# Optimization experiments

Measured on AMD Instinct MI355X. Metric: run time of the kernel, lower is better.

The kernel has to match this reference:

```python
import math
import jax, jax.numpy as jnp
import numpy as np

D_MODEL, N_HEADS, QKV, D_HEAD, D_FF, N_BLOCKS, IN_DIM = 288, 8, 328, 41, 1315, 4, 83
B, S = 1024, 128
EPS = 1e-5


def setup_inputs() -> dict:
    key = jax.random.key(0)
    ks = iter(jax.random.split(key, 64))
    def rn(shape, scale=0.05):
        return jax.random.normal(next(ks), shape, jnp.float32) * scale
    inp = {
        "x": jax.random.normal(next(ks), (B, S, IN_DIM), jnp.float32),
        "Wp": rn((D_MODEL, IN_DIM)), "bp": rn((D_MODEL,)),
        "phase": rn((D_MODEL,)),
        "Wq": rn((N_BLOCKS, QKV, D_MODEL)), "bq": rn((N_BLOCKS, QKV)),
        "Wk": rn((N_BLOCKS, QKV, D_MODEL)), "bk": rn((N_BLOCKS, QKV)),
        "Wv": rn((N_BLOCKS, QKV, D_MODEL)), "bv": rn((N_BLOCKS, QKV)),
        "Wo": rn((N_BLOCKS, D_MODEL, QKV)), "bo": rn((N_BLOCKS, D_MODEL)),
        "temp": jnp.ones((N_BLOCKS,), jnp.float32) + rn((N_BLOCKS,), 0.01),
        "qscale": jnp.ones((N_BLOCKS, N_HEADS), jnp.float32) + rn((N_BLOCKS, N_HEADS), 0.01),
        "Wf1": rn((N_BLOCKS, D_FF, D_MODEL)), "bf1": rn((N_BLOCKS, D_FF)),
        "Wf2": rn((N_BLOCKS, D_MODEL, D_FF)), "bf2": rn((N_BLOCKS, D_MODEL)),
        "n1w": jnp.ones((N_BLOCKS, D_MODEL), jnp.float32), "n1b": jnp.zeros((N_BLOCKS, D_MODEL), jnp.float32),
        "n2w": jnp.ones((N_BLOCKS, D_MODEL), jnp.float32), "n2b": jnp.zeros((N_BLOCKS, D_MODEL), jnp.float32),
        "skip": jnp.ones((N_BLOCKS,), jnp.float32),
        "bn_w": jnp.ones((D_MODEL,), jnp.float32), "bn_b": jnp.zeros((D_MODEL,), jnp.float32),
        "bn_mean": rn((D_MODEL,)), "bn_var": jax.random.uniform(next(ks), (D_MODEL,), jnp.float32, 0.5, 1.5),
        "h1w": rn((144, D_MODEL)), "h1b": rn((144,)),
        "h2w": rn((72, 144)), "h2b": rn((72,)),
        "h3w": rn((1, 72)), "h3b": rn((1,)),
        "u1w": rn((72, D_MODEL)), "u1b": rn((72,)),
        "u2w": rn((1, 72)), "u2b": rn((1,)),
    }
    return inp


def _layer_norm(x, w, b):
    mu = jnp.mean(x, axis=-1, keepdims=True)
    var = jnp.mean((x - mu) ** 2, axis=-1, keepdims=True)
    return (x - mu) * jax.lax.rsqrt(var + EPS) * w + b


def reference(x, Wp, bp, phase, Wq, bq, Wk, bk, Wv, bv, Wo, bo, temp, qscale,
              Wf1, bf1, Wf2, bf2, n1w, n1b, n2w, n2b, skip,
              bn_w, bn_b, bn_mean, bn_var,
              h1w, h1b, h2w, h2b, h3w, h3b, u1w, u1b, u2w, u2b):
    Bsz, Sl, _ = x.shape
    # input projection
    h = jnp.einsum('bsi,di->bsd', x, Wp) + bp
    # sinusoidal positional encoding modulated by cos(quantum_phase)
    pos = jnp.arange(Sl, dtype=jnp.float32)[:, None]
    div = jnp.exp(jnp.arange(0, D_MODEL, 2, dtype=jnp.float32) * (-math.log(10000.0) / D_MODEL))
    pe = jnp.zeros((Sl, D_MODEL), jnp.float32)
    pe = pe.at[:, 0::2].set(jnp.sin(pos * div)).at[:, 1::2].set(jnp.cos(pos * div))
    h = h + pe * jnp.cos(phase)

    for l in range(N_BLOCKS):
        # attention with temperature-scaled softmax + post-softmax per-head scale
        q = (jnp.einsum('bsd,qd->bsq', h, Wq[l]) + bq[l]).reshape(Bsz, Sl, N_HEADS, D_HEAD)
        k = (jnp.einsum('bsd,qd->bsq', h, Wk[l]) + bk[l]).reshape(Bsz, Sl, N_HEADS, D_HEAD)
        v = (jnp.einsum('bsd,qd->bsq', h, Wv[l]) + bv[l]).reshape(Bsz, Sl, N_HEADS, D_HEAD)
        scale = math.sqrt(D_HEAD) * temp[l]
        scores = jnp.einsum('bqhd,bkhd->bhqk', q, k) / scale  # [B,H,S,S]
        attn = jax.nn.softmax(scores, axis=-1) * qscale[l][None, :, None, None]
        o = jnp.einsum('bhqk,bkhd->bqhd', attn, v).reshape(Bsz, Sl, QKV)
        o = jnp.einsum('bsq,dq->bsd', o, Wo[l]) + bo[l]
        h = _layer_norm(h + skip[l] * o, n1w[l], n1b[l])
        # GELU FFN (exact erf gelu, dropout inactive in eval)
        f = jax.nn.gelu(jnp.einsum('bsd,fd->bsf', h, Wf1[l]) + bf1[l], approximate=False)
        f = jnp.einsum('bsf,df->bsd', f, Wf2[l]) + bf2[l]
        h = _layer_norm(h + f, n2w[l], n2b[l])

    pooled = jnp.mean(h, axis=1)  # [B, D_MODEL]
    # output head: BatchNorm1d (eval, running stats) -> GELU -> MLP
    z = (pooled - bn_mean) * jax.lax.rsqrt(bn_var + EPS) * bn_w + bn_b
    z = jax.nn.gelu(z, approximate=False)
    z = jax.nn.gelu(z @ h1w.T + h1b, approximate=False)
    z = jax.nn.gelu(z @ h2w.T + h2b, approximate=False)
    pred = z @ h3w.T + h3b  # [B, 1]
    # uncertainty head
    u = jax.nn.relu(pooled @ u1w.T + u1b)
    unc = jax.nn.softplus(u @ u2w.T + u2b)  # [B, 1]
    return pred, unc
```

## Files before the change

kernel.cpp:

```cpp
#include <hip/hip_runtime.h>
#include <cstdint>

typedef __attribute__((ext_vector_type(8))) short short8;
typedef __attribute__((ext_vector_type(4))) short s4v;
typedef __attribute__((ext_vector_type(4))) float floatx4;

#define DEV __device__ __forceinline__

DEV short f2bf(float f) {
  unsigned u = __builtin_bit_cast(unsigned, f);
  u += 0x7fffu + ((u >> 16) & 1u);
  return (short)(u >> 16);
}
DEV short f2bf_ru(float f) {
  unsigned u = __builtin_bit_cast(unsigned, f);
  return (short)((u + 0x8000u) >> 16);
}
DEV float bf2f(short s) {
  unsigned u = ((unsigned)(unsigned short)s) << 16;
  return __builtin_bit_cast(float, u);
}
DEV float gelu_exact(float x) {
  return 0.5f * x * (1.0f + erff(x * 0.70710678118654752f));
}
DEV float gelu_fast(float x) {
  const float t2 = 1.5957691216057308f * (x + 0.044715f * x * x * x);
  return x / (1.0f + __expf(-t2));
}
DEV void gload16(const void* g, void* l) {
  __builtin_amdgcn_global_load_lds((const __attribute__((address_space(1))) void*)g,
                                   (__attribute__((address_space(3))) void*)l,
                                   16, 0, 0);
}

template<int MODE>
__global__ __launch_bounds__(256)
void gemm_kernel(const short* __restrict__ A, const short* __restrict__ Bw,
                 const float* __restrict__ bias, short* __restrict__ C,
                 const float* __restrict__ pe,
                 int K, int lda, int ldb, int ldc, int Nstore, int NT, long hstride)
{
  __shared__ __align__(16) short lds[128 * 136];
  short* As = lds;
  short* Bs = lds + 128 * 32;
  short* Ct = lds;

  const int tid  = threadIdx.x;
  const int wave = tid >> 6, lane = tid & 63;
  const int quad = lane >> 4, r16 = lane & 15;
  const int per = gridDim.x >> 3;
  const int gti = (blockIdx.x & 7) * per + (blockIdx.x >> 3);
  const int mt = gti / NT, nt = gti - mt * NT;
  const int wm = (wave >> 1) * 64, wn = (wave & 1) * 64;

  const long Abase = (long)mt * 128 * lda;
  const long Bbase = (long)nt * 128 * ldb;

  const int row0 = tid >> 2,         cc0 = (tid & 3) ^ ((row0 >> 1) & 3);
  const int row1 = (256 + tid) >> 2, cc1 = ((256 + tid) & 3) ^ ((row1 >> 1) & 3);

  floatx4 acc[4][4] = {};

  for (int k0 = 0; k0 < K; k0 += 32) {
    __syncthreads();
    gload16(A  + Abase + (long)row0 * lda + k0 + cc0 * 8, &As[(0 * 256 + wave * 64) * 8]);
    gload16(A  + Abase + (long)row1 * lda + k0 + cc1 * 8, &As[(1 * 256 + wave * 64) * 8]);
    gload16(Bw + Bbase + (long)row0 * ldb + k0 + cc0 * 8, &Bs[(0 * 256 + wave * 64) * 8]);
    gload16(Bw + Bbase + (long)row1 * ldb + k0 + cc1 * 8, &Bs[(1 * 256 + wave * 64) * 8]);
    __syncthreads();

    short8 af[4], bfr[4];
#pragma unroll
    for (int i = 0; i < 4; ++i) {
      const int R = wm + i * 16 + r16;
      af[i] = *(const short8*)&As[R * 32 + (quad ^ ((R >> 1) & 3)) * 8];
    }
#pragma unroll
    for (int j = 0; j < 4; ++j) {
      const int R = wn + j * 16 + r16;
      bfr[j] = *(const short8*)&Bs[R * 32 + (quad ^ ((R >> 1) & 3)) * 8];
    }
#pragma unroll
    for (int i = 0; i < 4; ++i)
#pragma unroll
      for (int j = 0; j < 4; ++j)
        acc[i][j] = __builtin_amdgcn_mfma_f32_16x16x32_bf16(bfr[j], af[i], acc[i][j], 0, 0, 0);
  }

  const int mb0 = mt * 128, tb = nt * 128;

  __syncthreads();
#pragma unroll
  for (int j = 0; j < 4; ++j) {
    const int n0 = wn + j * 16 + quad * 4;
    const floatx4 b4 = *(const floatx4*)&bias[tb + n0];
#pragma unroll
    for (int i = 0; i < 4; ++i) {
      const int m = wm + i * 16 + r16;
      floatx4 v = acc[i][j] + b4;
      if (MODE == 1) {
#pragma unroll
        for (int rg = 0; rg < 4; ++rg) v[rg] = gelu_fast(v[rg]);
      }
      if (MODE == 2) {
        const floatx4 p4 = *(const floatx4*)&pe[((mb0 + m) & 127) * 384 + tb + n0];
        v = v + p4;
      }
      s4v o4;
#pragma unroll
      for (int rg = 0; rg < 4; ++rg) o4[rg] = f2bf_ru(v[rg]);
      *(s4v*)&Ct[m * 136 + n0] = o4;
    }
  }
  __syncthreads();

#pragma unroll
  for (int rr = 0; rr < 8; ++rr) {
    const int chunk = rr * 256 + tid;
    const int row = chunk >> 4, ch = chunk & 15;
    const int gcol = tb + ch * 8;
    if (MODE == 3) {
      const int g = gcol / 48, d0 = gcol - g * 48;
      *(short8*)(C + (long)g * hstride + (long)(mb0 + row) * 48 + d0) =
          *(const short8*)&Ct[row * 136 + ch * 8];
    } else if (gcol < Nstore) {
      *(short8*)(C + (long)(mb0 + row) * ldc + gcol) = *(const short8*)&Ct[row * 136 + ch * 8];
    }
  }
}

template<bool AHEAD>
__global__ __launch_bounds__(512, 4)
void gemm_ln_kernel(const short* __restrict__ A, const short* __restrict__ Bw,
                    const float* __restrict__ bias, short* __restrict__ h,
                    const float* __restrict__ lnw, const float* __restrict__ lnb,
                    const float* __restrict__ skip_p, int layer, int use_skip,
                    int K, int lda, int ldb, long ahs)
{
  __shared__ __align__(16) short lds[128 * 296];
  __shared__ float redp[4][2][2][16];
  __shared__ float reds[4][2][2][16];
  short* Hs = lds;

  const int tid  = threadIdx.x;
  const int wave = tid >> 6, lane = tid & 63;
  const int quad = lane >> 4, r16 = lane & 15;
  const int wr = wave >> 1, wc = wave & 1;
  const int mt = blockIdx.x;
  const long mrow0 = (long)mt * 128;

  floatx4 acc[2][9] = {};

  auto stage = [&](short* buf, int k0) {
    for (int c = tid; c < 1664; c += 512) {
      const void* src;
      if (c < 512) {
        const int row = c >> 2, cc = (c & 3) ^ ((row >> 1) & 3);
        if (AHEAD) {
          const int kc = k0 + cc * 8;
          const int g = kc / 48, d = kc - g * 48;
          src = A + (long)g * ahs + (mrow0 + row) * 48 + d;
        } else {
          src = A + (mrow0 + row) * lda + k0 + cc * 8;
        }
      } else {
        const int cb = c - 512;
        const int row = cb >> 2, cc = (cb & 3) ^ ((row >> 1) & 3);
        src = Bw + (long)row * ldb + k0 + cc * 8;
      }
      gload16(src, &buf[(size_t)(c & ~63) * 8]);
    }
  };

  auto compute = [&](const short* buf) {
    const short* As_ = buf;
    const short* Bs_ = buf + 4096;
    const int Ra0 = wr * 32 + r16, Ra1 = Ra0 + 16;
    const short8 af0 = *(const short8*)&As_[Ra0 * 32 + (quad ^ ((Ra0 >> 1) & 3)) * 8];
    const short8 af1 = *(const short8*)&As_[Ra1 * 32 + (quad ^ ((Ra1 >> 1) & 3)) * 8];
#pragma unroll
    for (int t = 0; t < 9; ++t) {
      const int Rb = wc * 144 + t * 16 + r16;
      const short8 b = *(const short8*)&Bs_[Rb * 32 + (quad ^ ((Rb >> 1) & 3)) * 8];
      acc[0][t] = __builtin_amdgcn_mfma_f32_16x16x32_bf16(b, af0, acc[0][t], 0, 0, 0);
      acc[1][t] = __builtin_amdgcn_mfma_f32_16x16x32_bf16(b, af1, acc[1][t], 0, 0, 0);
    }
  };

  short* const B0 = lds;
  short* const B1 = lds + 13312;

  stage(B0, 0);
  __syncthreads();
  int k0 = 0;
  while (true) {
    if (k0 + 32 < K) stage(B1, k0 + 32);
    compute(B0);
    __syncthreads();
    k0 += 32;
    if (k0 >= K) break;
    if (k0 + 32 < K) stage(B0, k0 + 32);
    compute(B1);
    __syncthreads();
    k0 += 32;
    if (k0 >= K) break;
  }

  for (int c = tid; c < 4608; c += 512) {
    const int row = c / 36, ch = c - row * 36;
    *(short8*)&Hs[row * 296 + ch * 8] =
        *(const short8*)(h + (mrow0 + row) * 288 + ch * 8);
  }
  __syncthreads();

  const float skipv = use_skip ? skip_p[layer] : 1.0f;
  const int m0 = wr * 32 + r16, m1 = m0 + 16;

  float ps0 = 0.f, ss0 = 0.f, ps1 = 0.f, ss1 = 0.f;
#pragma unroll
  for (int t = 0; t < 9; ++t) {
    const int n0 = wc * 144 + t * 16 + quad * 4;
    const floatx4 b4 = *(const floatx4*)&bias[n0];
    const s4v h40 = *(const s4v*)&Hs[m0 * 296 + n0];
    const s4v h41 = *(const s4v*)&Hs[m1 * 296 + n0];
#pragma unroll
    for (int rg = 0; rg < 4; ++rg) {
      const float y0 = bf2f(h40[rg]) + skipv * (acc[0][t][rg] + b4[rg]);
      const float y1 = bf2f(h41[rg]) + skipv * (acc[1][t][rg] + b4[rg]);
      acc[0][t][rg] = y0; acc[1][t][rg] = y1;
      ps0 += y0; ss0 += y0 * y0;
      ps1 += y1; ss1 += y1 * y1;
    }
  }
  ps0 += __shfl_xor(ps0, 16); ps0 += __shfl_xor(ps0, 32);
  ss0 += __shfl_xor(ss0, 16); ss0 += __shfl_xor(ss0, 32);
  ps1 += __shfl_xor(ps1, 16); ps1 += __shfl_xor(ps1, 32);
  ss1 += __shfl_xor(ss1, 16); ss1 += __shfl_xor(ss1, 32);
  if (lane < 16) {
    redp[wr][wc][0][r16] = ps0; redp[wr][wc][1][r16] = ps1;
    reds[wr][wc][0][r16] = ss0; reds[wr][wc][1][r16] = ss1;
  }
  __syncthreads();
  const float psum0 = redp[wr][0][0][r16] + redp[wr][1][0][r16];
  const float psum1 = redp[wr][0][1][r16] + redp[wr][1][1][r16];
  const float ssum0 = reds[wr][0][0][r16] + reds[wr][1][0][r16];
  const float ssum1 = reds[wr][0][1][r16] + reds[wr][1][1][r16];
  const float mean0 = psum0 * (1.f / 288.f), mean1 = psum1 * (1.f / 288.f);
  const float rstd0 = rsqrtf(ssum0 * (1.f / 288.f) - mean0 * mean0 + 1e-5f);
  const float rstd1 = rsqrtf(ssum1 * (1.f / 288.f) - mean1 * mean1 + 1e-5f);

#pragma unroll
  for (int t = 0; t < 9; ++t) {
    const int n0 = wc * 144 + t * 16 + quad * 4;
    const floatx4 w4 = *(const floatx4*)&lnw[n0];
    const floatx4 l4 = *(const floatx4*)&lnb[n0];
    s4v o0, o1;
#pragma unroll
    for (int rg = 0; rg < 4; ++rg) {
      o0[rg] = f2bf_ru((acc[0][t][rg] - mean0) * rstd0 * w4[rg] + l4[rg]);
      o1[rg] = f2bf_ru((acc[1][t][rg] - mean1) * rstd1 * w4[rg] + l4[rg]);
    }
    *(s4v*)&Hs[m0 * 296 + n0] = o0;
    *(s4v*)&Hs[m1 * 296 + n0] = o1;
  }
  __syncthreads();

  for (int c = tid; c < 4608; c += 512) {
    const int row = c / 36, ch = c - row * 36;
    *(short8*)(h + (mrow0 + row) * 288 + ch * 8) =
        *(const short8*)&Hs[row * 296 + ch * 8];
  }
}

__global__ __launch_bounds__(512, 2)
void ffn_kernel(short* __restrict__ h,
                const short* __restrict__ W1, const float* __restrict__ b1,
                const short* __restrict__ W2, const float* __restrict__ b2,
                const float* __restrict__ lnw, const float* __restrict__ lnb)
{
  __shared__ __align__(16) short lds[128 * 296];
  __shared__ float redp[4][2][2][16];
  __shared__ float reds[4][2][2][16];
  short* const fl = lds + 18432;

  const int tid  = threadIdx.x;
  const int wave = tid >> 6, lane = tid & 63;
  const int quad = lane >> 4, r16 = lane & 15;
  const int wr = wave >> 1, wp = wave & 1;
  const long mrow0 = (long)blockIdx.x * 128;

  short8 ha[2][9];
#pragma unroll
  for (int i = 0; i < 2; ++i) {
    const long rb = (mrow0 + wr * 32 + i * 16 + r16) * 288L;
#pragma unroll
    for (int k9 = 0; k9 < 9; ++k9)
      ha[i][k9] = *(const short8*)(h + rb + k9 * 32 + quad * 8);
  }

  floatx4 acc2[2][9] = {};

  const int srow = tid >> 2, scc = (tid & 3) ^ ((srow >> 1) & 3);

  auto stageW1 = [&](int c, int k9, short* dst) {
    gload16(W1 + ((long)(c * 128 + srow)) * 288 + k9 * 32 + scc * 8,
            &dst[(size_t)(tid & ~63) * 8]);
  };
  auto stageW2 = [&](int c, int ks, short* dst) {
    for (int c2 = tid; c2 < 1152; c2 += 512) {
      const int row = c2 >> 2, cc = (c2 & 3) ^ ((row >> 1) & 3);
      gload16(W2 + (long)row * 1408 + c * 128 + ks * 32 + cc * 8,
              &dst[(size_t)(c2 & ~63) * 8]);
    }
  };

  stageW1(0, 0, lds);
  __syncthreads();
  int cur = 0;

  for (int c = 0; c < 11; ++c) {
    floatx4 acc1[2][4] = {};

#pragma unroll
    for (int k9 = 0; k9 < 9; ++k9) {
      short* const Sn = lds + (cur ^ 1) * 9216;
      if (k9 < 8) stageW1(c, k9 + 1, Sn);
      else        stageW2(c, 0, Sn);

      const short* Sc = lds + cur * 9216;
      short8 bfr[4];
#pragma unroll
      for (int j = 0; j < 4; ++j) {
        const int R = wp * 64 + j * 16 + r16;
        bfr[j] = *(const short8*)&Sc[R * 32 + (quad ^ ((R >> 1) & 3)) * 8];
      }
#pragma unroll
      for (int i = 0; i < 2; ++i)
#pragma unroll
        for (int j = 0; j < 4; ++j)
          acc1[i][j] = __builtin_amdgcn_mfma_f32_16x16x32_bf16(bfr[j], ha[i][k9], acc1[i][j], 0, 0, 0);

      if (k9 == 8) {
#pragma unroll
        for (int i = 0; i < 2; ++i) {
          const int m = wr * 32 + i * 16 + r16;
#pragma unroll
          for (int j = 0; j < 4; ++j) {
            const int nb = c * 128 + wp * 64 + j * 16 + quad * 4;
            const floatx4 b4 = *(const floatx4*)&b1[nb];
            s4v o;
#pragma unroll
            for (int rg = 0; rg < 4; ++rg)
              o[rg] = f2bf_ru(gelu_fast(acc1[i][j][rg] + b4[rg]));
            const int ks = wp * 2 + (j >> 1);
            const int mg = ((j & 1) * 2 + (quad >> 1)) ^ ((m >> 1) & 3);
            *(s4v*)&fl[ks * 4096 + m * 32 + mg * 8 + (quad & 1) * 4] = o;
          }
        }
      }
      __syncthreads();
      cur ^= 1;
    }

#pragma unroll
    for (int ks = 0; ks < 4; ++ks) {
      short* const Sn = lds + (cur ^ 1) * 9216;
      if (ks < 3)      stageW2(c, ks + 1, Sn);
      else if (c < 10) stageW1(c + 1, 0, Sn);

      const short* Sc = lds + cur * 9216;
      short8 af2[2], br[9];
#pragma unroll
      for (int i = 0; i < 2; ++i) {
        const int R = wr * 32 + i * 16 + r16;
        af2[i] = *(const short8*)&fl[ks * 4096 + R * 32 + (quad ^ ((R >> 1) & 3)) * 8];
      }
#pragma unroll
      for (int t = 0; t < 9; ++t) {
        const int R = wp * 144 + t * 16 + r16;
        br[t] = *(const short8*)&Sc[R * 32 + (quad ^ ((R >> 1) & 3)) * 8];
      }
#pragma unroll
      for (int i = 0; i < 2; ++i)
#pragma unroll
        for (int t = 0; t < 9; ++t)
          acc2[i][t] = __builtin_amdgcn_mfma_f32_16x16x32_bf16(br[t], af2[i], acc2[i][t], 0, 0, 0);

      __syncthreads();
      cur ^= 1;
    }
  }

  for (int c2 = tid; c2 < 4608; c2 += 512) {
    const int row = c2 / 36, ch = c2 - row * 36;
    *(short8*)&lds[row * 296 + ch * 8] =
        *(const short8*)(h + (mrow0 + row) * 288 + ch * 8);
  }
  __syncthreads();

  const int m0 = wr * 32 + r16, m1 = m0 + 16;
  float ps0 = 0.f, ss0 = 0.f, ps1 = 0.f, ss1 = 0.f;
#pragma unroll
  for (int t = 0; t < 9; ++t) {
    const int n0 = wp * 144 + t * 16 + quad * 4;
    const floatx4 b4 = *(const floatx4*)&b2[n0];
    const s4v h40 = *(const s4v*)&lds[m0 * 296 + n0];
    const s4v h41 = *(const s4v*)&lds[m1 * 296 + n0];
#pragma unroll
    for (int rg = 0; rg < 4; ++rg) {
      const float y0 = bf2f(h40[rg]) + acc2[0][t][rg] + b4[rg];
      const float y1 = bf2f(h41[rg]) + acc2[1][t][rg] + b4[rg];
      acc2[0][t][rg] = y0; acc2[1][t][rg] = y1;
      ps0 += y0; ss0 += y0 * y0;
      ps1 += y1; ss1 += y1 * y1;
    }
  }
  ps0 += __shfl_xor(ps0, 16); ps0 += __shfl_xor(ps0, 32);
  ss0 += __shfl_xor(ss0, 16); ss0 += __shfl_xor(ss0, 32);
  ps1 += __shfl_xor(ps1, 16); ps1 += __shfl_xor(ps1, 32);
  ss1 += __shfl_xor(ss1, 16); ss1 += __shfl_xor(ss1, 32);
  if (lane < 16) {
    redp[wr][wp][0][r16] = ps0; redp[wr][wp][1][r16] = ps1;
    reds[wr][wp][0][r16] = ss0; reds[wr][wp][1][r16] = ss1;
  }
  __syncthreads();
  const float psum0 = redp[wr][0][0][r16] + redp[wr][1][0][r16];
  const float psum1 = redp[wr][0][1][r16] + redp[wr][1][1][r16];
  const float ssum0 = reds[wr][0][0][r16] + reds[wr][1][0][r16];
  const float ssum1 = reds[wr][0][1][r16] + reds[wr][1][1][r16];
  const float mean0 = psum0 * (1.f / 288.f), mean1 = psum1 * (1.f / 288.f);
  const float rstd0 = rsqrtf(ssum0 * (1.f / 288.f) - mean0 * mean0 + 1e-5f);
  const float rstd1 = rsqrtf(ssum1 * (1.f / 288.f) - mean1 * mean1 + 1e-5f);

#pragma unroll
  for (int t = 0; t < 9; ++t) {
    const int n0 = wp * 144 + t * 16 + quad * 4;
    const floatx4 w4 = *(const floatx4*)&lnw[n0];
    const floatx4 l4 = *(const floatx4*)&lnb[n0];
    s4v o0, o1;
#pragma unroll
    for (int rg = 0; rg < 4; ++rg) {
      o0[rg] = f2bf_ru((acc2[0][t][rg] - mean0) * rstd0 * w4[rg] + l4[rg]);
      o1[rg] = f2bf_ru((acc2[1][t][rg] - mean1) * rstd1 * w4[rg] + l4[rg]);
    }
    *(s4v*)&lds[m0 * 296 + n0] = o0;
    *(s4v*)&lds[m1 * 296 + n0] = o1;
  }
  __syncthreads();

  for (int c2 = tid; c2 < 4608; c2 += 512) {
    const int row = c2 / 36, ch = c2 - row * 36;
    *(short8*)(h + (mrow0 + row) * 288 + ch * 8) =
        *(const short8*)&lds[row * 296 + ch * 8];
  }
}

__global__ __launch_bounds__(256)
void attn_kernel(short* __restrict__ qkv,
                 const float* __restrict__ qscale, int layer, long Mc)
{
  __shared__ __align__(16) short qk[2 * 128 * 72];
  __shared__ __align__(16) short vsT[48 * 136 + 32];
  __shared__ float red[2][2][64];

  short* qs = qk;
  short* ks = qk + 128 * 72;
  short* Pb = qk;

  const int b = blockIdx.x, h = blockIdx.y;
  const int tid = threadIdx.x;
  const long sec = Mc * 48;
  const short* qg = qkv + (long)h * sec + (long)b * 128 * 48;
  const short* kg = qg + 8 * sec;
  const short* vg = qg + 16 * sec;
  short* og = qkv + (long)(16 + h) * sec + (long)b * 128 * 48;

  for (int c = tid; c < 768; c += 256) {
    const int s = c / 6, dc = c - (c / 6) * 6;
    *(short8*)&qs[s * 72 + dc * 8] = *(const short8*)(qg + (long)s * 48 + dc * 8);
    *(short8*)&ks[s * 72 + dc * 8] = *(const short8*)(kg + (long)s * 48 + dc * 8);
  }
  {
    short8 z;
#pragma unroll
    for (int j = 0; j < 8; ++j) z[j] = 0;
    for (int c = tid; c < 384; c += 256) {
      const int s = c / 3, t = c - (c / 3) * 3;
      *(short8*)&qs[s * 72 + 48 + t * 8] = z;
      *(short8*)&ks[s * 72 + 48 + t * 8] = z;
    }
  }
  for (int c = tid; c < 768; c += 256) {
    const int s = c & 127, dc = c >> 7;
    const short8 tv = *(const short8*)(vg + (long)s * 48 + dc * 8);
#pragma unroll
    for (int j = 0; j < 8; ++j) {
      const int row = dc * 8 + j;
      vsT[row * 136 + ((row >> 3) & 3) * 8 + s] = tv[j];
    }
  }
  __syncthreads();

  const int wave = tid >> 6, lane = tid & 63;
  const int quad = lane >> 4, r16 = lane & 15;
  const int wm = (wave >> 1) * 64, wn = (wave & 1) * 64;
  const int rh = wave >> 1, ch = wave & 1;
  const float qsc = qscale[layer * 8 + h];

  floatx4 acc[4][4] = {};
#pragma unroll
  for (int kk = 0; kk < 2; ++kk) {
    const int k0 = kk * 32;
    short8 af[4], bfr[4];
#pragma unroll
    for (int i = 0; i < 4; ++i)
      af[i] = *(const short8*)&qs[(wm + i * 16 + r16) * 72 + k0 + quad * 8];
#pragma unroll
    for (int j = 0; j < 4; ++j)
      bfr[j] = *(const short8*)&ks[(wn + j * 16 + r16) * 72 + k0 + quad * 8];
#pragma unroll
    for (int i = 0; i < 4; ++i)
#pragma unroll
      for (int j = 0; j < 4; ++j)
        acc[i][j] = __builtin_amdgcn_mfma_f32_16x16x32_bf16(bfr[j], af[i], acc[i][j], 0, 0, 0);
  }

  float rmax[4], rsum[4];
#pragma unroll
  for (int i = 0; i < 4; ++i) {
    float m = acc[i][0][0];
#pragma unroll
    for (int j = 0; j < 4; ++j)
#pragma unroll
      for (int rg = 0; rg < 4; ++rg) m = fmaxf(m, acc[i][j][rg]);
    m = fmaxf(m, __shfl_xor(m, 16));
    m = fmaxf(m, __shfl_xor(m, 32));
    rmax[i] = m;
  }
  if (lane < 16)
#pragma unroll
    for (int i = 0; i < 4; ++i) red[rh][ch][i * 16 + r16] = rmax[i];
  __syncthreads();
#pragma unroll
  for (int i = 0; i < 4; ++i)
    rmax[i] = fmaxf(red[rh][0][i * 16 + r16], red[rh][1][i * 16 + r16]);

#pragma unroll
  for (int i = 0; i < 4; ++i) {
    float s = 0.f;
#pragma unroll
    for (int j = 0; j < 4; ++j)
#pragma unroll
      for (int rg = 0; rg < 4; ++rg) {
        const float e = __expf(acc[i][j][rg] - rmax[i]);
        acc[i][j][rg] = e;
        s += e;
      }
    s += __shfl_xor(s, 16);
    s += __shfl_xor(s, 32);
    rsum[i] = s;
  }
  __syncthreads();
  if (lane < 16)
#pragma unroll
    for (int i = 0; i < 4; ++i) red[rh][ch][i * 16 + r16] = rsum[i];
  __syncthreads();
#pragma unroll
  for (int i = 0; i < 4; ++i)
    rmax[i] = qsc / (red[rh][0][i * 16 + r16] + red[rh][1][i * 16 + r16]);

#pragma unroll
  for (int i = 0; i < 4; ++i) {
    const int sq = wm + i * 16 + r16;
#pragma unroll
    for (int j = 0; j < 4; ++j) {
      const int sk0 = wn + j * 16 + quad * 4;
      s4v p4;
#pragma unroll
      for (int rg = 0; rg < 4; ++rg) p4[rg] = f2bf_ru(acc[i][j][rg] * rmax[i]);
      *(s4v*)&Pb[sq * 136 + sk0] = p4;
    }
  }
  __syncthreads();

  const int om = (wave >> 1) * 64, on = (wave & 1) * 32;
  const int jn = (on == 0) ? 2 : 1;
  floatx4 oacc[4][2] = {};
  for (int kk = 0; kk < 4; ++kk) {
    const int k0 = kk * 32;
    short8 af[4], bfr[2];
#pragma unroll
    for (int i = 0; i < 4; ++i)
      af[i] = *(const short8*)&Pb[(om + i * 16 + r16) * 136 + k0 + quad * 8];
    for (int j = 0; j < jn; ++j) {
      const int row = on + j * 16 + r16;
      bfr[j] = *(const short8*)&vsT[row * 136 + ((row >> 3) & 3) * 8 + k0 + quad * 8];
    }
#pragma unroll
    for (int i = 0; i < 4; ++i)
      for (int j = 0; j < jn; ++j)
        oacc[i][j] = __builtin_amdgcn_mfma_f32_16x16x32_bf16(bfr[j], af[i], oacc[i][j], 0, 0, 0);
  }
#pragma unroll
  for (int i = 0; i < 4; ++i)
    for (int j = 0; j < jn; ++j) {
      const int d0 = on + j * 16 + quad * 4;
      const int sq = om + i * 16 + r16;
      s4v o4;
#pragma unroll
      for (int rg = 0; rg < 4; ++rg) o4[rg] = f2bf_ru(oacc[i][j][rg]);
      *(s4v*)(og + (long)sq * 48 + d0) = o4;
    }
}

__global__ __launch_bounds__(256)
void head_kernel(const short* __restrict__ hb, float* __restrict__ out,
                 const float* bn_w, const float* bn_b, const float* bn_mean, const float* bn_var,
                 const float* h1w, const float* h1b, const float* h2w, const float* h2b,
                 const float* h3w, const float* h3b,
                 const float* u1w, const float* u1b, const float* u2w, const float* u2b)
{
  __shared__ float psum[252][8];
  __shared__ float pooled[288], z[288], z1[144], z2[72], uu[72];
  const int b = blockIdx.x, tid = threadIdx.x;

  if (tid < 252) {
    const int cch = tid % 36, grp = tid / 36;
    float a[8];
#pragma unroll
    for (int j = 0; j < 8; ++j) a[j] = 0.f;
    for (int r = grp; r < 128; r += 7) {
      const short8 hv = *(const short8*)(hb + ((long)b * 128 + r) * 288 + cch * 8);
#pragma unroll
      for (int j = 0; j < 8; ++j) a[j] += bf2f(hv[j]);
    }
#pragma unroll
    for (int j = 0; j < 8; ++j) psum[tid][j] = a[j];
  }
  __syncthreads();
  for (int d = tid; d < 288; d += 256) {
    const int cch = d >> 3, j = d & 7;
    float s = 0.f;
#pragma unroll
    for (int g = 0; g < 7; ++g) s += psum[g * 36 + cch][j];
    pooled[d] = s * (1.f / 128.f);
  }
  __syncthreads();

  for (int d = tid; d < 288; d += 256) {
    const float p = pooled[d];
    z[d] = gelu_exact((p - bn_mean[d]) * rsqrtf(bn_var[d] + 1e-5f) * bn_w[d] + bn_b[d]);
  }
  __syncthreads();

  if (tid < 144) {
    float s = h1b[tid];
    for (int k = 0; k < 288; ++k) s += z[k] * h1w[tid * 288 + k];
    z1[tid] = gelu_exact(s);
  } else if (tid < 216) {
    const int t = tid - 144;
    float s = u1b[t];
    for (int k = 0; k < 288; ++k) s += pooled[k] * u1w[t * 288 + k];
    uu[t] = fmaxf(s, 0.f);
  }
  __syncthreads();

  if (tid < 72) {
    float s = h2b[tid];
    for (int k = 0; k < 144; ++k) s += z1[k] * h2w[tid * 144 + k];
    z2[tid] = gelu_exact(s);
  }
  __syncthreads();

  if (tid == 0) {
    float s = h3b[0];
    for (int k = 0; k < 72; ++k) s += z2[k] * h3w[k];
    out[b] = s;
  }
  if (tid == 64) {
    float s = u2b[0];
    for (int k = 0; k < 72; ++k) s += uu[k] * u2w[k];
    out[1024 + b] = (s > 20.f) ? s : log1pf(__expf(s));
  }
}

__global__ void conv_w_kernel(const float* __restrict__ src, short* __restrict__ dst,
                              int N, int K, int Npad, int Kpad, int total)
{
  const int i = blockIdx.x * 256 + threadIdx.x;
  if (i >= total) return;
  const int kk = i % Kpad;
  const int t  = i / Kpad;
  const int n  = t % Npad;
  const int l  = t / Npad;
  const float v = (n < N && kk < K) ? src[((long)l * N + n) * K + kk] : 0.f;
  dst[i] = f2bf(v);
}

__global__ void conv_b_kernel(const float* __restrict__ src, float* __restrict__ dst,
                              int N, int Npad, int total)
{
  const int i = blockIdx.x * 256 + threadIdx.x;
  if (i >= total) return;
  const int n = i % Npad, l = i / Npad;
  dst[i] = (n < N) ? src[l * N + n] : 0.f;
}

__global__ void conv_wqkv_kernel(const float* __restrict__ Wq, const float* __restrict__ Wk,
                                 const float* __restrict__ Wv, const float* __restrict__ temp,
                                 short* __restrict__ dst)
{
  const int i = blockIdx.x * 256 + threadIdx.x;
  if (i >= 4 * 1152 * 288) return;
  const int kk = i % 288;
  const int t  = i / 288;
  const int r  = t % 1152;
  const int l  = t / 1152;
  const int g  = r / 48, d = r - (r / 48) * 48;
  const int sec = g >> 3, head = g & 7;
  float v = 0.f;
  if (d < 41) {
    const float* W = (sec == 0) ? Wq : (sec == 1) ? Wk : Wv;
    v = W[((long)l * 328 + head * 41 + d) * 288 + kk];
    if (sec == 0) v *= 1.0f / (6.4031242374328485f * temp[l]);
  }
  dst[i] = f2bf(v);
}

__global__ void conv_bqkv_kernel(const float* __restrict__ bq, const float* __restrict__ bk,
                                 const float* __restrict__ bv, const float* __restrict__ temp,
                                 float* __restrict__ dst)
{
  const int i = blockIdx.x * 256 + threadIdx.x;
  if (i >= 4 * 1152) return;
  const int r = i % 1152, l = i / 1152;
  const int g = r / 48, d = r - (r / 48) * 48;
  const int sec = g >> 3, head = g & 7;
  float v = 0.f;
  if (d < 41) {
    const float* b = (sec == 0) ? bq : (sec == 1) ? bk : bv;
    v = b[l * 328 + head * 41 + d];
    if (sec == 0) v *= 1.0f / (6.4031242374328485f * temp[l]);
  }
  dst[i] = v;
}

__global__ void conv_wo_kernel(const float* __restrict__ Wo, short* __restrict__ dst)
{
  const int i = blockIdx.x * 256 + threadIdx.x;
  if (i >= 4 * 288 * 384) return;
  const int kk = i % 384;
  const int t  = i / 384;
  const int n  = t % 288;
  const int l  = t / 288;
  const int head = kk / 48, d = kk - head * 48;
  float v = 0.f;
  if (d < 41) v = Wo[((long)l * 288 + n) * 328 + head * 41 + d];
  dst[i] = f2bf(v);
}

__global__ void conv_x_kernel(const float* __restrict__ x, short* __restrict__ xb, int total)
{
  const int i = blockIdx.x * 256 + threadIdx.x;
  if (i >= total) return;
  const int c = i % 96;
  const int r = i / 96;
  xb[i] = f2bf((c < 83) ? x[(long)r * 83 + c] : 0.f);
}

__global__ void pe_kernel(const float* __restrict__ phase, float* __restrict__ pe_mod)
{
  const int i = blockIdx.x * 256 + threadIdx.x;
  if (i >= 128 * 384) return;
  const int d = i % 384, s = i / 384;
  float out = 0.f;
  if (d < 288) {
    const int pair = d >> 1;
    const float divv = expf((float)(2 * pair) * (-9.210340371976184f / 288.f));
    const float arg = (float)s * divv;
    const float v = (d & 1) ? cosf(arg) : sinf(arg);
    out = v * cosf(phase[d]);
  }
  pe_mod[i] = out;
}

extern "C" void kernel_launch(void* const* d_in, const int* in_sizes, int n_in,
                              void* d_out, int out_size, void* d_ws, size_t ws_size,
                              hipStream_t stream)
{
  (void)in_sizes; (void)n_in; (void)out_size;

  const float* x     = (const float*)d_in[0];
  const float* Wp    = (const float*)d_in[1];
  const float* bp    = (const float*)d_in[2];
  const float* phase = (const float*)d_in[3];
  const float* Wq    = (const float*)d_in[4];
  const float* bq    = (const float*)d_in[5];
  const float* Wk    = (const float*)d_in[6];
  const float* bk    = (const float*)d_in[7];
  const float* Wv    = (const float*)d_in[8];
  const float* bv    = (const float*)d_in[9];
  const float* Wo    = (const float*)d_in[10];
  const float* bo    = (const float*)d_in[11];
  const float* temp  = (const float*)d_in[12];
  const float* qscale= (const float*)d_in[13];
  const float* Wf1   = (const float*)d_in[14];
  const float* bf1   = (const float*)d_in[15];
  const float* Wf2   = (const float*)d_in[16];
  const float* bf2   = (const float*)d_in[17];
  const float* n1w   = (const float*)d_in[18];
  const float* n1b   = (const float*)d_in[19];
  const float* n2w   = (const float*)d_in[20];
  const float* n2b   = (const float*)d_in[21];
  const float* skip  = (const float*)d_in[22];
  const float* bn_w  = (const float*)d_in[23];
  const float* bn_b  = (const float*)d_in[24];
  const float* bn_mean=(const float*)d_in[25];
  const float* bn_var= (const float*)d_in[26];
  const float* h1w   = (const float*)d_in[27];
  const float* h1b   = (const float*)d_in[28];
  const float* h2w   = (const float*)d_in[29];
  const float* h2b   = (const float*)d_in[30];
  const float* h3w   = (const float*)d_in[31];
  const float* h3b   = (const float*)d_in[32];
  const float* u1w   = (const float*)d_in[33];
  const float* u1b   = (const float*)d_in[34];
  const float* u2w   = (const float*)d_in[35];
  const float* u2b   = (const float*)d_in[36];

  char* ws = (char*)d_ws;
  size_t off = 0;
  auto alloc = [&](size_t n) -> char* {
    off = (off + 255) & ~(size_t)255;
    char* p = ws + off;
    off += n;
    return p;
  };

  const long M = 131072;

  short* h_bf   = (short*)alloc((size_t)M * 288 * 2);
  float* pe_mod = (float*)alloc(128 * 384 * 4);

  short* Wp_b   = (short*)alloc((size_t)384 * 96 * 2);
  short* Wqkv_b = (short*)alloc((size_t)4 * 1152 * 288 * 2);
  short* Wo_b   = (short*)alloc((size_t)4 * 288 * 384 * 2);
  short* Wf1_b  = (short*)alloc((size_t)4 * 1408 * 288 * 2);
  short* Wf2_b  = (short*)alloc((size_t)4 * 384 * 1408 * 2);

  float* bp_p   = (float*)alloc((size_t)384 * 4);
  float* bqkv_p = (float*)alloc((size_t)4 * 1152 * 4);
  float* bo_p   = (float*)alloc((size_t)4 * 384 * 4);
  float* bf1_p  = (float*)alloc((size_t)4 * 1408 * 4);
  float* bf2_p  = (float*)alloc((size_t)4 * 384 * 4);

  const size_t fixed = off;
  int NC = 1;
  while (NC < 16 && fixed + (size_t)(M / NC) * 2304 + (1u << 20) > ws_size) NC <<= 1;
  const long Mc = M / NC;
  const long sec = Mc * 48;

  char* R = alloc((size_t)Mc * 2304);
  short* qkv_bf = (short*)R;
  short* x_bfc  = (short*)R;

  const dim3 blk(256);

  auto conv_w = [&](const float* s, short* d, int N, int K, int Np, int Kp, int L) {
    const int total = L * Np * Kp;
    conv_w_kernel<<<dim3((total + 255) / 256), blk, 0, stream>>>(s, d, N, K, Np, Kp, total);
  };
  auto conv_b = [&](const float* s, float* d, int N, int Np, int L) {
    const int total = L * Np;
    conv_b_kernel<<<dim3((total + 255) / 256), blk, 0, stream>>>(s, d, N, Np, total);
  };
  conv_w(Wp,  Wp_b,  288,   83, 384,   96, 1);
  conv_wqkv_kernel<<<dim3((4 * 1152 * 288 + 255) / 256), blk, 0, stream>>>(Wq, Wk, Wv, temp, Wqkv_b);
  conv_wo_kernel<<<dim3((4 * 288 * 384 + 255) / 256), blk, 0, stream>>>(Wo, Wo_b);
  conv_w(Wf1, Wf1_b, 1315, 288, 1408, 288, 4);
  conv_w(Wf2, Wf2_b, 288, 1315, 384, 1408, 4);
  conv_b(bp,  bp_p,  288,  384, 1);
  conv_bqkv_kernel<<<dim3((4 * 1152 + 255) / 256), blk, 0, stream>>>(bq, bk, bv, temp, bqkv_p);
  conv_b(bo,  bo_p,  288,  384, 4);
  conv_b(bf1, bf1_p, 1315, 1408, 4);
  conv_b(bf2, bf2_p, 288,  384, 4);
  pe_kernel<<<dim3((128 * 384 + 255) / 256), blk, 0, stream>>>(phase, pe_mod);

  auto gemm = [&](int mode, const short* A, const short* Bmat, const float* bias,
                  short* C, const float* pe, int K, int lda, int ldb, int ldc,
                  int Nstore, int NT, long Mrows, long hstride) {
    const dim3 grid((unsigned)((Mrows / 128) * NT));
    switch (mode) {
      case 0: gemm_kernel<0><<<grid, blk, 0, stream>>>(A, Bmat, bias, C, pe, K, lda, ldb, ldc, Nstore, NT, hstride); break;
      case 1: gemm_kernel<1><<<grid, blk, 0, stream>>>(A, Bmat, bias, C, pe, K, lda, ldb, ldc, Nstore, NT, hstride); break;
      case 2: gemm_kernel<2><<<grid, blk, 0, stream>>>(A, Bmat, bias, C, pe, K, lda, ldb, ldc, Nstore, NT, hstride); break;
      default: gemm_kernel<3><<<grid, blk, 0, stream>>>(A, Bmat, bias, C, pe, K, lda, ldb, ldc, Nstore, NT, hstride); break;
    }
  };

  for (int c = 0; c < NC; ++c) {
    const float* x_c = x + (size_t)c * Mc * 83;
    short* h_c = h_bf + (size_t)c * Mc * 288;

    const int xtot = (int)(Mc * 96);
    conv_x_kernel<<<dim3((xtot + 255) / 256), blk, 0, stream>>>(x_c, x_bfc, xtot);

    gemm(2, x_bfc, Wp_b, bp_p, h_c, pe_mod, 96, 96, 96, 288, 288, 3, Mc, 0);

    for (int l = 0; l < 4; ++l) {
      const short* Wqkv_l = Wqkv_b + (size_t)l * 1152 * 288;
      const short* Wo_l   = Wo_b   + (size_t)l * 288 * 384;
      const short* Wf1_l  = Wf1_b  + (size_t)l * 1408 * 288;
      const short* Wf2_l  = Wf2_b  + (size_t)l * 384 * 1408;

      gemm(3, h_c, Wqkv_l, bqkv_p + l * 1152, qkv_bf, nullptr,
           288, 288, 288, 0, 1152, 9, Mc, sec);

      attn_kernel<<<dim3((unsigned)(Mc / 128), 8), blk, 0, stream>>>(
          qkv_bf, qscale, l, Mc);

      gemm_ln_kernel<true><<<dim3((unsigned)(Mc / 128)), dim3(512), 0, stream>>>(
          qkv_bf + 16 * sec, Wo_l, bo_p + l * 384, h_c, n1w + l * 288, n1b + l * 288,
          skip, l, 1, 384, 48, 384, sec);

      ffn_kernel<<<dim3((unsigned)(Mc / 128)), dim3(512), 0, stream>>>(
          h_c, Wf1_l, bf1_p + l * 1408, Wf2_l, bf2_p + l * 384,
          n2w + l * 288, n2b + l * 288);
    }
  }

  head_kernel<<<dim3(1024), blk, 0, stream>>>(h_bf, (float*)d_out,
      bn_w, bn_b, bn_mean, bn_var,
      h1w, h1b, h2w, h2b, h3w, h3b,
      u1w, u1b, u2w, u2b);
}
```

Measured before the change: 3.492 ms.

## Double K-step to 64 per LDS stage in GEMM and FFN kernels

Both the generic GEMM and the fused FFN kernel now stage 64-wide K slices into LDS per barrier pair instead of 32-wide, using a new XOR swizzle for the 64-column layout. The GEMM keeps a 32-wide tail path for leftover K. This halves the number of __syncthreads and staging rounds per tile. The trade is a larger LDS footprint in the FFN kernel (about 106KB), which may limit occupancy at two blocks per CU, plus more complex indexing.

```diff
diff --git a/kernel.cpp b/kernel.cpp
--- a/kernel.cpp
+++ b/kernel.cpp
@@ -31,6 +31,13 @@
   __builtin_amdgcn_global_load_lds((const __attribute__((address_space(1))) void*)g,
                                    (__attribute__((address_space(3))) void*)l,
                                    16, 0, 0);
+}
+
+DEV int stage_col64(int row, int g) {
+  return ((g >> 2) ^ (row & 1)) * 32 + (((g & 3) ^ ((row >> 1) & 3))) * 8;
+}
+DEV int frag_off64(int R, int s, int quad) {
+  return R * 64 + ((((s ^ (R & 1)) << 2) | (quad ^ ((R >> 1) & 3)))) * 8;
 }
 
 template<int MODE>
@@ -41,8 +48,6 @@
                  int K, int lda, int ldb, int ldc, int Nstore, int NT, long hstride)
 {
   __shared__ __align__(16) short lds[128 * 136];
-  short* As = lds;
-  short* Bs = lds + 128 * 32;
   short* Ct = lds;
 
   const int tid  = threadIdx.x;
@@ -56,12 +61,49 @@
   const long Abase = (long)mt * 128 * lda;
   const long Bbase = (long)nt * 128 * ldb;
 
-  const int row0 = tid >> 2,         cc0 = (tid & 3) ^ ((row0 >> 1) & 3);
-  const int row1 = (256 + tid) >> 2, cc1 = ((256 + tid) & 3) ^ ((row1 >> 1) & 3);
-
   floatx4 acc[4][4] = {};
 
-  for (int k0 = 0; k0 < K; k0 += 32) {
+  int k0 = 0;
+  for (; k0 + 64 <= K; k0 += 64) {
+    __syncthreads();
+#pragma unroll
+    for (int j = 0; j < 8; ++j) {
+      const int c2 = tid + j * 256;
+      const int cb = c2 & 1023;
+      const int row = cb >> 3, g = cb & 7;
+      const int col = stage_col64(row, g);
+      const short* src = (c2 < 1024) ? (A  + Abase + (long)row * lda + k0 + col)
+                                     : (Bw + Bbase + (long)row * ldb + k0 + col);
+      gload16(src, &lds[(size_t)(c2 & ~63) * 8]);
+    }
+    __syncthreads();
+
+#pragma unroll
+    for (int s = 0; s < 2; ++s) {
+      short8 af[4], bfr[4];
+#pragma unroll
+      for (int i = 0; i < 4; ++i) {
+        const int R = wm + i * 16 + r16;
+        af[i] = *(const short8*)&lds[frag_off64(R, s, quad)];
+      }
+#pragma unroll
+      for (int j = 0; j < 4; ++j) {
+        const int R = wn + j * 16 + r16;
+        bfr[j] = *(const short8*)&lds[8192 + frag_off64(R, s, quad)];
+      }
+#pragma unroll
+      for (int i = 0; i < 4; ++i)
+#pragma unroll
+        for (int j = 0; j < 4; ++j)
+          acc[i][j] = __builtin_amdgcn_mfma_f32_16x16x32_bf16(bfr[j], af[i], acc[i][j], 0, 0, 0);
+    }
+  }
+
+  if (k0 < K) {
+    short* As = lds;
+    short* Bs = lds + 128 * 32;
+    const int row0 = tid >> 2,         cc0 = (tid & 3) ^ ((row0 >> 1) & 3);
+    const int row1 = (256 + tid) >> 2, cc1 = ((256 + tid) & 3) ^ ((row1 >> 1) & 3);
     __syncthreads();
     gload16(A  + Abase + (long)row0 * lda + k0 + cc0 * 8, &As[(0 * 256 + wave * 64) * 8]);
     gload16(A  + Abase + (long)row1 * lda + k0 + cc1 * 8, &As[(1 * 256 + wave * 64) * 8]);
@@ -278,10 +320,10 @@
                 const short* __restrict__ W2, const float* __restrict__ b2,
                 const float* __restrict__ lnw, const float* __restrict__ lnb)
 {
-  __shared__ __align__(16) short lds[128 * 296];
+  __shared__ __align__(16) short lds[53248];
   __shared__ float redp[4][2][2][16];
   __shared__ float reds[4][2][2][16];
-  short* const fl = lds + 18432;
+  short* const fl = lds + 36864;
 
   const int tid  = threadIdx.x;
   const int wave = tid >> 6, lane = tid & 63;
@@ -300,21 +342,36 @@
 
   floatx4 acc2[2][9] = {};
 
-  const int srow = tid >> 2, scc = (tid & 3) ^ ((srow >> 1) & 3);
-
-  auto stageW1 = [&](int c, int k9, short* dst) {
-    gload16(W1 + ((long)(c * 128 + srow)) * 288 + k9 * 32 + scc * 8,
+  auto stageW1_64 = [&](int c, int kp, short* dst) {
+#pragma unroll
+    for (int j = 0; j < 2; ++j) {
+      const int c2 = tid + j * 512;
+      const int row = c2 >> 3, g = c2 & 7;
+      gload16(W1 + ((long)(c * 128 + row)) * 288 + kp * 64 + stage_col64(row, g),
+              &dst[(size_t)(c2 & ~63) * 8]);
+    }
+  };
+  auto stageW1_32 = [&](int c, int k9, short* dst) {
+    const int row = tid >> 2, cc = (tid & 3) ^ ((row >> 1) & 3);
+    gload16(W1 + ((long)(c * 128 + row)) * 288 + k9 * 32 + cc * 8,
             &dst[(size_t)(tid & ~63) * 8]);
   };
-  auto stageW2 = [&](int c, int ks, short* dst) {
-    for (int c2 = tid; c2 < 1152; c2 += 512) {
-      const int row = c2 >> 2, cc = (c2 & 3) ^ ((row >> 1) & 3);
-      gload16(W2 + (long)row * 1408 + c * 128 + ks * 32 + cc * 8,
-              &dst[(size_t)(c2 & ~63) * 8]);
+  auto stageW2_64 = [&](int c, int kh, short* dst) {
+#pragma unroll
+    for (int j = 0; j < 5; ++j) {
+      const int c2 = tid + j * 512;
+      if (c2 < 2304) {
+        const int row = c2 >> 3, g = c2 & 7;
+        gload16(W2 + (long)row * 1408 + c * 128 + kh * 64 + stage_col64(row, g),
+                &dst[(size_t)(c2 & ~63) * 8]);
+      }
     }
   };
 
-  stageW1(0, 0, lds);
+  short* const ring0 = lds;
+  short* const ring1 = lds + 18432;
+
+  stageW1_64(0, 0, ring0);
   __syncthreads();
   int cur = 0;
 
@@ -322,12 +379,35 @@
     floatx4 acc1[2][4] = {};
 
 #pragma unroll
-    for (int k9 = 0; k9 < 9; ++k9) {
-      short* const Sn = lds + (cur ^ 1) * 9216;
-      if (k9 < 8) stageW1(c, k9 + 1, Sn);
-      else        stageW2(c, 0, Sn);
-
-      const short* Sc = lds + cur * 9216;
+    for (int kp = 0; kp < 4; ++kp) {
+      short* const Sn = cur ? ring0 : ring1;
+      const short* Sc = cur ? ring1 : ring0;
+      if (kp < 3) stageW1_64(c, kp + 1, Sn);
+      else        stageW1_32(c, 8, Sn);
+
+#pragma unroll
+      for (int s = 0; s < 2; ++s) {
+        short8 bfr[4];
+#pragma unroll
+        for (int j = 0; j < 4; ++j) {
+          const int R = wp * 64 + j * 16 + r16;
+          bfr[j] = *(const short8*)&Sc[frag_off64(R, s, quad)];
+        }
+#pragma unroll
+        for (int i = 0; i < 2; ++i)
+#pragma unroll
+          for (int j = 0; j < 4; ++j)
+            acc1[i][j] = __builtin_amdgcn_mfma_f32_16x16x32_bf16(bfr[j], ha[i][kp * 2 + s], acc1[i][j], 0, 0, 0);
+      }
+      __syncthreads();
+      cur ^= 1;
+    }
+
+    {
+      short* const Sn = cur ? ring0 : ring1;
+      const short* Sc = cur ? ring1 : ring0;
+      stageW2_64(c, 0, Sn);
+
       short8 bfr[4];
 #pragma unroll
       for (int j = 0; j < 4; ++j) {
@@ -338,24 +418,22 @@
       for (int i = 0; i < 2; ++i)
 #pragma unroll
         for (int j = 0; j < 4; ++j)
-          acc1[i][j] = __builtin_amdgcn_mfma_f32_16x16x32_bf16(bfr[j], ha[i][k9], acc1[i][j], 0, 0, 0);
-
-      if (k9 == 8) {
-#pragma unroll
-        for (int i = 0; i < 2; ++i) {
-          const int m = wr * 32 + i * 16 + r16;
-#pragma unroll
-          for (int j = 0; j < 4; ++j) {
-            const int nb = c * 128 + wp * 64 + j * 16 + quad * 4;
-            const floatx4 b4 = *(const floatx4*)&b1[nb];
-            s4v o;
-#pragma unroll
-            for (int rg = 0; rg < 4; ++rg)
-              o[rg] = f2bf_ru(gelu_fast(acc1[i][j][rg] + b4[rg]));
-            const int ks = wp * 2 + (j >> 1);
-            const int mg = ((j & 1) * 2 + (quad >> 1)) ^ ((m >> 1) & 3);
-            *(s4v*)&fl[ks * 4096 + m * 32 + mg * 8 + (quad & 1) * 4] = o;
-          }
+          acc1[i][j] = __builtin_amdgcn_mfma_f32_16x16x32_bf16(bfr[j], ha[i][8], acc1[i][j], 0, 0, 0);
+
+#pragma unroll
+      for (int i = 0; i < 2; ++i) {
+        const int m = wr * 32 + i * 16 + r16;
+#pragma unroll
+        for (int j = 0; j < 4; ++j) {
+          const int nb = c * 128 + wp * 64 + j * 16 + quad * 4;
+          const floatx4 b4 = *(const floatx4*)&b1[nb];
+          s4v o;
+#pragma unroll
+          for (int rg = 0; rg < 4; ++rg)
+            o[rg] = f2bf_ru(gelu_fast(acc1[i][j][rg] + b4[rg]));
+          const int ks = wp * 2 + (j >> 1);
+          const int mg = ((j & 1) * 2 + (quad >> 1)) ^ ((m >> 1) & 3);
+          *(s4v*)&fl[ks * 4096 + m * 32 + mg * 8 + (quad & 1) * 4] = o;
         }
       }
       __syncthreads();
@@ -363,29 +441,33 @@
     }
 
 #pragma unroll
-    for (int ks = 0; ks < 4; ++ks) {
-      short* const Sn = lds + (cur ^ 1) * 9216;
-      if (ks < 3)      stageW2(c, ks + 1, Sn);
-      else if (c < 10) stageW1(c + 1, 0, Sn);
-
-      const short* Sc = lds + cur * 9216;
-      short8 af2[2], br[9];
-#pragma unroll
-      for (int i = 0; i < 2; ++i) {
-        const int R = wr * 32 + i * 16 + r16;
-        af2[i] = *(const short8*)&fl[ks * 4096 + R * 32 + (quad ^ ((R >> 1) & 3)) * 8];
+    for (int sg = 0; sg < 2; ++sg) {
+      short* const Sn = cur ? ring0 : ring1;
+      const short* Sc = cur ? ring1 : ring0;
+      if (sg == 0)     stageW2_64(c, 1, Sn);
+      else if (c < 10) stageW1_64(c + 1, 0, Sn);
+
+#pragma unroll
+      for (int s = 0; s < 2; ++s) {
+        const int ks = sg * 2 + s;
+        short8 af2[2];
+#pragma unroll
+        for (int i = 0; i < 2; ++i) {
+          const int R = wr * 32 + i * 16 + r16;
+          af2[i] = *(const short8*)&fl[ks * 4096 + R * 32 + (quad ^ ((R >> 1) & 3)) * 8];
+        }
+        short8 br[9];
+#pragma unroll
+        for (int t = 0; t < 9; ++t) {
+          const int R = wp * 144 + t * 16 + r16;
+          br[t] = *(const short8*)&Sc[frag_off64(R, s, quad)];
+        }
+#pragma unroll
+        for (int i = 0; i < 2; ++i)
+#pragma unroll
+          for (int t = 0; t < 9; ++t)
+            acc2[i][t] = __builtin_amdgcn_mfma_f32_16x16x32_bf16(br[t], af2[i], acc2[i][t], 0, 0, 0);
       }
-#pragma unroll
-      for (int t = 0; t < 9; ++t) {
-        const int R = wp * 144 + t * 16 + r16;
-        br[t] = *(const short8*)&Sc[R * 32 + (quad ^ ((R >> 1) & 3)) * 8];
-      }
-#pragma unroll
-      for (int i = 0; i < 2; ++i)
-#pragma unroll
-        for (int t = 0; t < 9; ++t)
-          acc2[i][t] = __builtin_amdgcn_mfma_f32_16x16x32_bf16(br[t], af2[i], acc2[i][t], 0, 0, 0);
-
       __syncthreads();
       cur ^= 1;
     }
```

After: 3.145 ms. 10.0% less time.
